# Kernel tuning notes

Measured on AMD Instinct MI355X. Metric: run time of the kernel, lower is better.

## Reference

```python
import jax, jax.numpy as jnp
import numpy as np

G, N_PER_G, V, H, DIN, DOUT, E = 1024, 64, 32, 128, 128, 10, 1048576
N = G * N_PER_G


def _lin(key, fan_in, fan_out):
    k1, k2 = jax.random.split(key)
    s = 1.0 / np.sqrt(fan_in)
    return (jax.random.uniform(k1, (fan_in, fan_out), jnp.float32, -s, s),
            jax.random.uniform(k2, (fan_out,), jnp.float32, -s, s))


def setup_inputs() -> dict:
    key = jax.random.key(0)
    ks = jax.random.split(key, 16)
    x = jax.random.normal(ks[0], (N, DIN), jnp.float32)
    # random edges constrained within each graph's contiguous node block
    gid = jax.random.randint(ks[1], (E,), 0, G)
    src = gid * N_PER_G + jax.random.randint(ks[2], (E,), 0, N_PER_G)
    dst = gid * N_PER_G + jax.random.randint(ks[3], (E,), 0, N_PER_G)
    edge_index = jnp.stack([src, dst]).astype(jnp.int64)
    batch = jnp.repeat(jnp.arange(G, dtype=jnp.int64), N_PER_G)
    edge_weights = jnp.ones((G, N_PER_G, V), jnp.float32) / V  # uniform init
    vemb = jax.random.normal(ks[4], (G, V, H), jnp.float32)
    vemb = vemb / jnp.linalg.norm(vemb, axis=-1, keepdims=True)
    W_emb, b_emb = _lin(ks[5], DIN, H)
    W_gcn, b_gcn = _lin(ks[6], H, H)
    aff_W1, aff_b1 = _lin(ks[7], H, H)
    aff_W2, aff_b2 = _lin(ks[8], H, H)
    vn_W1, vn_b1 = _lin(ks[9], H, H)
    vn_W2, vn_b2 = _lin(ks[10], H, H)
    mlp_W1, mlp_b1 = _lin(ks[11], H, H)
    mlp_W2, mlp_b2 = _lin(ks[12], H, DOUT)
    return dict(x=x, edge_index=edge_index, batch=batch, edge_weights=edge_weights,
                vemb=vemb, W_emb=W_emb, b_emb=b_emb, W_gcn=W_gcn, b_gcn=b_gcn,
                aff_W1=aff_W1, aff_b1=aff_b1, aff_W2=aff_W2, aff_b2=aff_b2,
                vn_W1=vn_W1, vn_b1=vn_b1, vn_W2=vn_W2, vn_b2=vn_b2,
                mlp_W1=mlp_W1, mlp_b1=mlp_b1, mlp_W2=mlp_W2, mlp_b2=mlp_b2)


def reference(x, edge_index, batch, edge_weights, vemb, W_emb, b_emb, W_gcn, b_gcn,
              aff_W1, aff_b1, aff_W2, aff_b2, vn_W1, vn_b1, vn_W2, vn_b2,
              mlp_W1, mlp_b1, mlp_W2, mlp_b2):
    n_nodes = x.shape[0]
    g, n, v = edge_weights.shape
    h = x @ W_emb + b_emb                                   # node embedding
    # GCNConv with self-loops and symmetric normalization
    hw = h @ W_gcn
    sl = jnp.arange(n_nodes)
    s = jnp.concatenate([edge_index[0], sl])
    d = jnp.concatenate([edge_index[1], sl])
    deg = jax.ops.segment_sum(jnp.ones_like(d, dtype=h.dtype), d, num_segments=n_nodes)
    inv = jax.lax.rsqrt(jnp.maximum(deg, 1.0))
    msg = hw[s] * (inv[s] * inv[d])[:, None]                # [E+N, H]
    h = jax.nn.relu(jax.ops.segment_sum(msg, d, num_segments=n_nodes) + b_gcn)
    # affinity MLP
    aff = jax.nn.relu(h @ aff_W1 + aff_b1) @ aff_W2 + aff_b2
    hg = h.reshape(g, n, -1)
    affg = aff.reshape(g, n, -1)
    # attention vs fixed normalized virtual-node embeddings
    att = jnp.einsum('gnh,gvh->gnv', affg, vemb) / jnp.sqrt(jnp.asarray(hg.shape[-1], h.dtype))
    ew = edge_weights * (1.0 + jax.nn.sigmoid(att))
    rs = ew.sum(axis=-1, keepdims=True)
    ew = ew / jnp.where(rs == 0, 1.0, rs)                   # row-normalize
    vn = jnp.einsum('gnv,gnh->gvh', ew, hg)                 # weighted scatter-pool
    vn = jax.nn.relu(vn @ vn_W1 + vn_b1) @ vn_W2 + vn_b2
    gf = vn.mean(axis=1)                                    # [G, H]
    return jax.nn.relu(gf @ mlp_W1 + mlp_b1) @ mlp_W2 + mlp_b2
```

## Files before the change

### kernel.cpp

```cpp
#include <hip/hip_runtime.h>
#include <hip/hip_bf16.h>
#include <cstddef>


#define EDGES 1048576
#define TS 72
#define AS 64
#define VS 136
#define BS 40

typedef __attribute__((ext_vector_type(8))) short short8;
typedef __attribute__((ext_vector_type(4))) float f32x4;
typedef __hip_bfloat16 bf;
struct __align__(8) bf4 { bf v[4]; };

__device__ __forceinline__ int foff(int nt, int ks, int l15, int kofs) {
    return (nt * 4 + ks) * 512 + l15 * 32 + kofs;
}

__device__ __forceinline__ short8 cvt8(const float* p) {
    float4 v0 = *(const float4*)p, v1 = *(const float4*)(p + 4);
    union { short8 v; bf e[8]; } u;
    u.e[0] = __float2bfloat16(v0.x); u.e[1] = __float2bfloat16(v0.y);
    u.e[2] = __float2bfloat16(v0.z); u.e[3] = __float2bfloat16(v0.w);
    u.e[4] = __float2bfloat16(v1.x); u.e[5] = __float2bfloat16(v1.y);
    u.e[6] = __float2bfloat16(v1.z); u.e[7] = __float2bfloat16(v1.w);
    return u.v;
}

__global__ __launch_bounds__(256) void prep(
    const float* __restrict__ vemb, const float* __restrict__ aff_b2,
    const float* __restrict__ aff_W2, const float* __restrict__ W_emb,
    const float* __restrict__ W_gcn, const float* __restrict__ b_emb,
    const float* __restrict__ aff_W1, const float* __restrict__ vn_W1,
    const float* __restrict__ vn_W2,
    bf* __restrict__ gWb, float* __restrict__ bfold,
    bf* __restrict__ gS, float* __restrict__ gbatt, unsigned* __restrict__ Cnt)
{
    const int b = blockIdx.x, t = threadIdx.x;
    const int wv = t >> 6, lane = t & 63, l15 = lane & 15, q = lane >> 4;
    const int kofs = q * 8;
    if (b < 1024) {
        __shared__ __align__(16) bf sV[32 * VS];
        const float4* gv = (const float4*)(vemb + (size_t)b * 4096);
#pragma unroll
        for (int tt = 0; tt < 4; ++tt) {
            int i = t + tt * 256;
            int v = i >> 5, o4 = i & 31;
            float4 w = gv[i];
            bf4 tv;
            tv.v[0] = __float2bfloat16(w.x); tv.v[1] = __float2bfloat16(w.y);
            tv.v[2] = __float2bfloat16(w.z); tv.v[3] = __float2bfloat16(w.w);
            *(bf4*)(sV + v * VS + o4 * 4) = tv;
        }
        __syncthreads();
        {
            int v = t >> 3, sg = t & 7;
            float s = 0.f;
            const bf* pv = sV + v * VS + sg * 16;
            const float* pb = aff_b2 + sg * 16;
#pragma unroll
            for (int o = 0; o < 16; ++o) s += pb[o] * __bfloat162float(pv[o]);
            s += __shfl_xor(s, 1); s += __shfl_xor(s, 2); s += __shfl_xor(s, 4);
            if (sg == 0) gbatt[b * 32 + v] = s;
        }
        {
            const int mt = wv & 1, nb = (wv >> 1) * 4;
            f32x4 acc[4] = {};
#pragma unroll
            for (int ks = 0; ks < 4; ++ks) {
                short8 a = *(const short8*)(sV + (mt * 16 + l15) * VS + ks * 32 + kofs);
#pragma unroll
                for (int nt = 0; nt < 4; ++nt) {
                    int n = (nb + nt) * 16 + l15;
                    short8 bb = cvt8(aff_W2 + n * 128 + ks * 32 + kofs);
                    acc[nt] = __builtin_amdgcn_mfma_f32_16x16x32_bf16(a, bb, acc[nt], 0, 0, 0);
                }
            }
#pragma unroll
            for (int nt = 0; nt < 4; ++nt)
#pragma unroll
                for (int r = 0; r < 4; ++r) {
                    int v = mt * 16 + q * 4 + r;
                    int k = (nb + nt) * 16 + l15;
                    int off = ((v >> 4) * 4 + (k >> 5)) * 512 + (v & 15) * 32 + (k & 31);
                    gS[(size_t)b * 4096 + off] = __float2bfloat16(acc[nt][r]);
                }
        }
    } else if (b == 1024) {
        if (t < 128) {
            float acc = 0.f;
#pragma unroll 16
            for (int m = 0; m < 128; ++m) acc = fmaf(b_emb[m], W_gcn[m * 128 + t], acc);
            bfold[t] = acc;
        }
#pragma unroll
        for (int kt2 = 0; kt2 < 2; ++kt2) {
            int kt = wv * 2 + kt2;
            short8 Af[4];
#pragma unroll
            for (int ks = 0; ks < 4; ++ks)
                Af[ks] = cvt8(W_emb + (kt * 16 + l15) * 128 + ks * 32 + kofs);
#pragma unroll
            for (int jt = 0; jt < 8; ++jt) {
                f32x4 acc = {};
#pragma unroll
                for (int ks = 0; ks < 4; ++ks) {
                    union { short8 v; bf e[8]; } u;
#pragma unroll
                    for (int i = 0; i < 8; ++i)
                        u.e[i] = __float2bfloat16(W_gcn[(ks * 32 + kofs + i) * 128 + jt * 16 + l15]);
                    acc = __builtin_amdgcn_mfma_f32_16x16x32_bf16(Af[ks], u.v, acc, 0, 0, 0);
                }
#pragma unroll
                for (int r = 0; r < 4; ++r) {
                    int k = kt * 16 + q * 4 + r;
                    gWb[(jt * 4 + (k >> 5)) * 512 + l15 * 32 + (k & 31)] =
                        __float2bfloat16(acc[r]);
                }
            }
        }
    } else if (b < 1028) {
        const float* src = (b == 1025) ? aff_W1 : (b == 1026) ? vn_W1 : vn_W2;
        bf* dst = gWb + (size_t)(b - 1024) * 16384;
        for (int i = t; i < 16384; i += 256) {
            int n = i >> 7, k = i & 127;
            int off = ((n >> 4) * 4 + (k >> 5)) * 512 + (n & 15) * 32 + (k & 31);
            dst[off] = __float2bfloat16(src[k * 128 + n]);
        }
    } else {
        for (int i = t; i < 1024; i += 256) Cnt[i] = 0u;
    }
}

__global__ __launch_bounds__(256) void scat(const int* __restrict__ ei,
                                            unsigned* __restrict__ Cnt,
                                            unsigned short* __restrict__ sorted)
{
    __shared__ unsigned lh[1024];
    __shared__ unsigned sBase[1024];
    int t = threadIdx.x, b = blockIdx.x;
    for (int i = t; i < 1024; i += 256) lh[i] = 0;
    __syncthreads();
    unsigned er[16];
    int base = b * 4096;
#pragma unroll
    for (int i = 0; i < 16; ++i) {
        int e = base + i * 256 + t;
        int s = ei[e], d = ei[EDGES + e];
        unsigned g = (unsigned)s >> 6;
        er[i] = (g << 12) | (unsigned)((d & 63) << 6) | (unsigned)(s & 63);
        atomicAdd(&lh[g], 1u);
    }
    __syncthreads();
    for (int i = t; i < 1024; i += 256) {
        unsigned c = lh[i];
        if (c) sBase[i] = atomicAdd(&Cnt[i], c);
    }
    __syncthreads();
    for (int i = t; i < 1024; i += 256) lh[i] = 0;
    __syncthreads();
#pragma unroll
    for (int i = 0; i < 16; ++i) {
        unsigned g = er[i] >> 12;
        unsigned r = atomicAdd(&lh[g], 1u);
        unsigned p = sBase[g] + r;
        if (p < 2048) sorted[(size_t)g * 2048 + p] = (unsigned short)(er[i] & 0xFFFu);
    }
}

__device__ __forceinline__ void gemmA8(const short8 A[4], const bf* __restrict__ gW,
                                       int l15, int kofs, f32x4 acc[8])
{
#pragma unroll
    for (int hf = 0; hf < 2; ++hf) {
        short8 b[4], bn[4];
#pragma unroll
        for (int nt = 0; nt < 4; ++nt)
            b[nt] = *(const short8*)(gW + foff(hf * 4 + nt, 0, l15, kofs));
#pragma unroll
        for (int ks = 0; ks < 4; ++ks) {
            if (ks < 3)
#pragma unroll
                for (int nt = 0; nt < 4; ++nt)
                    bn[nt] = *(const short8*)(gW + foff(hf * 4 + nt, ks + 1, l15, kofs));
#pragma unroll
            for (int nt = 0; nt < 4; ++nt)
                acc[hf * 4 + nt] = __builtin_amdgcn_mfma_f32_16x16x32_bf16(
                    A[ks], b[nt], acc[hf * 4 + nt], 0, 0, 0);
#pragma unroll
            for (int nt = 0; nt < 4; ++nt) b[nt] = bn[nt];
        }
    }
}

__device__ __forceinline__ void gemmA4(const short8 A[4], const bf* __restrict__ gW,
                                       int ntb, int l15, int kofs, f32x4 acc[4])
{
    short8 b[4], bn[4];
#pragma unroll
    for (int nt = 0; nt < 4; ++nt)
        b[nt] = *(const short8*)(gW + foff(ntb + nt, 0, l15, kofs));
#pragma unroll
    for (int ks = 0; ks < 4; ++ks) {
        if (ks < 3)
#pragma unroll
            for (int nt = 0; nt < 4; ++nt)
                bn[nt] = *(const short8*)(gW + foff(ntb + nt, ks + 1, l15, kofs));
#pragma unroll
        for (int nt = 0; nt < 4; ++nt)
            acc[nt] = __builtin_amdgcn_mfma_f32_16x16x32_bf16(A[ks], b[nt], acc[nt], 0, 0, 0);
#pragma unroll
        for (int nt = 0; nt < 4; ++nt) b[nt] = bn[nt];
    }
}

__device__ __forceinline__ void bounceA(const float vals[8][4], bf* slab,
                                        int q, int l15, short8 A[4])
{
#pragma unroll
    for (int ks = 0; ks < 4; ++ks) {
#pragma unroll
        for (int h = 0; h < 2; ++h)
#pragma unroll
            for (int r = 0; r < 4; ++r)
                slab[(q * 4 + r) * BS + h * 16 + l15] = __float2bfloat16(vals[ks * 2 + h][r]);
        A[ks] = *(const short8*)(slab + l15 * BS + q * 8);
    }
}

__global__ __launch_bounds__(256, 4) void fused_graph(
    const float* __restrict__ x, const float* __restrict__ edge_w,
    const bf* __restrict__ gWb, const float* __restrict__ bfold,
    const float* __restrict__ b_gcn, const float* __restrict__ aff_b1,
    const float* __restrict__ vn_b1, const float* __restrict__ vn_b2,
    const bf* __restrict__ gS, const float* __restrict__ gbatt,
    const float* __restrict__ mlp_W1, const float* __restrict__ mlp_b1,
    const float* __restrict__ mlp_W2, const float* __restrict__ mlp_b2,
    const unsigned short* __restrict__ sorted, const unsigned* __restrict__ Cnt,
    float* __restrict__ out)
{
    __shared__ __align__(16) bf sT [128 * TS];
    __shared__ __align__(16) bf sAdj[64 * AS];
    __shared__ __align__(16) bf sBounce[4 * 16 * BS];
    __shared__ __align__(16) bf sVn[32 * VS];
    __shared__ float sInv[64];

    const int tid = threadIdx.x;
    const int g = blockIdx.x;
    const int wv = tid >> 6;
    const int lane = tid & 63;
    const int l15 = lane & 15;
    const int q = lane >> 4;
    const int kofs = q * 8;
    bf* slab = sBounce + wv * (16 * BS);
    float* sGfp = (float*)sBounce;
    unsigned* cnt = (unsigned*)sVn;

    {
        uint4* c4 = (uint4*)cnt;
        c4[tid] = make_uint4(0, 0, 0, 0);
    }
    __syncthreads();
    {
        unsigned ecnt = Cnt[g]; if (ecnt > 2048) ecnt = 2048;
        const unsigned short* seg = sorted + (size_t)g * 2048;
        for (unsigned i = tid; i < ecnt; i += 256) {
            unsigned w = seg[i];
            atomicAdd(&cnt[(w >> 6) * 16 + ((w & 63u) >> 2)], 1u << ((w & 3u) * 8));
        }
    }
    __syncthreads();
    {
        int row = tid >> 2, q4 = tid & 3;
        float rs = 0.f;
#pragma unroll
        for (int w4 = 0; w4 < 4; ++w4) {
            unsigned wd = cnt[row * 16 + q4 * 4 + w4];
            bf4 tv;
#pragma unroll
            for (int j = 0; j < 4; ++j) {
                int c = (q4 * 4 + w4) * 4 + j;
                float v = (float)((wd >> (j * 8)) & 255u) + (c == row ? 1.f : 0.f);
                rs += v;
                tv.v[j] = __float2bfloat16(v);
            }
            *(bf4*)(sAdj + row * AS + (q4 * 4 + w4) * 4) = tv;
        }
        rs += __shfl_xor(rs, 1);
        rs += __shfl_xor(rs, 2);
        if (q4 == 0) sInv[row] = rsqrtf(rs);
    }
    __syncthreads();

    {
        const float4* xrow = (const float4*)(x + ((size_t)g * 64 + 16 * wv + l15) * 128);
        short8 A[4];
#pragma unroll
        for (int ks = 0; ks < 4; ++ks) {
            float4 a0 = xrow[ks * 8 + q * 2];
            float4 a1 = xrow[ks * 8 + q * 2 + 1];
            union { short8 v; bf e[8]; } u;
            u.e[0] = __float2bfloat16(a0.x); u.e[1] = __float2bfloat16(a0.y);
            u.e[2] = __float2bfloat16(a0.z); u.e[3] = __float2bfloat16(a0.w);
            u.e[4] = __float2bfloat16(a1.x); u.e[5] = __float2bfloat16(a1.y);
            u.e[6] = __float2bfloat16(a1.z); u.e[7] = __float2bfloat16(a1.w);
            A[ks] = u.v;
        }
        f32x4 acc[8] = {};
        gemmA8(A, gWb, l15, kofs, acc);
        float bf_[8];
#pragma unroll
        for (int nt = 0; nt < 8; ++nt) bf_[nt] = bfold[nt * 16 + l15];
        float iv[4];
#pragma unroll
        for (int r = 0; r < 4; ++r) iv[r] = sInv[16 * wv + q * 4 + r];
#pragma unroll
        for (int nt = 0; nt < 8; ++nt) {
            bf4 tv;
#pragma unroll
            for (int r = 0; r < 4; ++r)
                tv.v[r] = __float2bfloat16((acc[nt][r] + bf_[nt]) * iv[r]);
            *(bf4*)(sT + (nt * 16 + l15) * TS + 16 * wv + q * 4) = tv;
        }
    }
    __syncthreads();

    float hvals[8][4];
    {
        f32x4 acc[8] = {};
#pragma unroll
        for (int ks = 0; ks < 2; ++ks) {
            short8 a = *(const short8*)(sAdj + (16 * wv + l15) * AS + ks * 32 + kofs);
#pragma unroll
            for (int nt = 0; nt < 8; ++nt) {
                short8 bb = *(const short8*)(sT + (nt * 16 + l15) * TS + ks * 32 + kofs);
                acc[nt] = __builtin_amdgcn_mfma_f32_16x16x32_bf16(a, bb, acc[nt], 0, 0, 0);
            }
        }
        float iv[4];
#pragma unroll
        for (int r = 0; r < 4; ++r) iv[r] = sInv[16 * wv + q * 4 + r];
#pragma unroll
        for (int nt = 0; nt < 8; ++nt) {
            float bg = b_gcn[nt * 16 + l15];
#pragma unroll
            for (int r = 0; r < 4; ++r)
                hvals[nt][r] = fmaxf(acc[nt][r] * iv[r] + bg, 0.f);
        }
    }
    __syncthreads();

    short8 Ah[4];
    {
#pragma unroll
        for (int nt = 0; nt < 8; ++nt) {
            bf4 tv;
#pragma unroll
            for (int r = 0; r < 4; ++r) tv.v[r] = __float2bfloat16(hvals[nt][r]);
            *(bf4*)(sT + (nt * 16 + l15) * TS + 16 * wv + q * 4) = tv;
        }
        bounceA(hvals, slab, q, l15, Ah);
    }

    short8 Aa[4];
    {
        f32x4 acc[8] = {};
        gemmA8(Ah, gWb + 16384, l15, kofs, acc);
        float av[8][4];
#pragma unroll
        for (int nt = 0; nt < 8; ++nt) {
            float ba = aff_b1[nt * 16 + l15];
#pragma unroll
            for (int r = 0; r < 4; ++r) av[nt][r] = fmaxf(acc[nt][r] + ba, 0.f);
        }
        bounceA(av, slab, q, l15, Aa);
    }

    {
        short8 Sf[8];
#pragma unroll
        for (int nt = 0; nt < 2; ++nt)
#pragma unroll
            for (int ks = 0; ks < 4; ++ks)
                Sf[nt * 4 + ks] = *(const short8*)(gS + (size_t)g * 4096 + foff(nt, ks, l15, kofs));
        float ewv[2][4];
#pragma unroll
        for (int nt = 0; nt < 2; ++nt)
#pragma unroll
            for (int r = 0; r < 4; ++r)
                ewv[nt][r] = edge_w[(size_t)g * 2048 + (16 * wv + q * 4 + r) * 32 + nt * 16 + l15];
        float bt[2] = { gbatt[g * 32 + l15], gbatt[g * 32 + 16 + l15] };
        f32x4 acc[2] = {};
#pragma unroll
        for (int ks = 0; ks < 4; ++ks) {
            acc[0] = __builtin_amdgcn_mfma_f32_16x16x32_bf16(Aa[ks], Sf[ks],     acc[0], 0, 0, 0);
            acc[1] = __builtin_amdgcn_mfma_f32_16x16x32_bf16(Aa[ks], Sf[4 + ks], acc[1], 0, 0, 0);
        }
        const float sc = 0.08838834764831845f;
        float e[2][4];
#pragma unroll
        for (int r = 0; r < 4; ++r) {
#pragma unroll
            for (int nt = 0; nt < 2; ++nt) {
                float att = (acc[nt][r] + bt[nt]) * sc;
                e[nt][r] = ewv[nt][r] * (1.f + 1.f / (1.f + __expf(-att)));
            }
            float rs = e[0][r] + e[1][r];
            rs += __shfl_xor(rs, 1); rs += __shfl_xor(rs, 2);
            rs += __shfl_xor(rs, 4); rs += __shfl_xor(rs, 8);
            float ri = (rs == 0.f) ? 1.f : 1.f / rs;
            e[0][r] *= ri; e[1][r] *= ri;
        }
#pragma unroll
        for (int nt = 0; nt < 2; ++nt) {
            bf4 tv;
#pragma unroll
            for (int r = 0; r < 4; ++r) tv.v[r] = __float2bfloat16(e[nt][r]);
            *(bf4*)(sAdj + (nt * 16 + l15) * AS + 16 * wv + q * 4) = tv;
        }
    }
    __syncthreads();

    const int mb = wv & 1, hf = wv >> 1;
    {
        f32x4 acc[4] = {};
#pragma unroll
        for (int ks = 0; ks < 2; ++ks) {
            short8 a = *(const short8*)(sAdj + (mb * 16 + l15) * AS + ks * 32 + kofs);
#pragma unroll
            for (int nt = 0; nt < 4; ++nt) {
                short8 bb = *(const short8*)(sT + (hf * 64 + nt * 16 + l15) * TS + ks * 32 + kofs);
                acc[nt] = __builtin_amdgcn_mfma_f32_16x16x32_bf16(a, bb, acc[nt], 0, 0, 0);
            }
        }
#pragma unroll
        for (int nt = 0; nt < 4; ++nt)
#pragma unroll
            for (int r = 0; r < 4; ++r)
                sVn[(mb * 16 + q * 4 + r) * VS + hf * 64 + nt * 16 + l15] =
                    __float2bfloat16(acc[nt][r]);
    }
    __syncthreads();

    bf* vn1 = sT;
    {
        short8 A[4];
#pragma unroll
        for (int ks = 0; ks < 4; ++ks)
            A[ks] = *(const short8*)(sVn + (mb * 16 + l15) * VS + ks * 32 + kofs);
        f32x4 acc[4] = {};
        gemmA4(A, gWb + 2 * 16384, hf * 4, l15, kofs, acc);
#pragma unroll
        for (int nt = 0; nt < 4; ++nt) {
            float b1 = vn_b1[hf * 64 + nt * 16 + l15];
#pragma unroll
            for (int r = 0; r < 4; ++r)
                vn1[(mb * 16 + q * 4 + r) * VS + hf * 64 + nt * 16 + l15] =
                    __float2bfloat16(fmaxf(acc[nt][r] + b1, 0.f));
        }
    }
    __syncthreads();

    {
        short8 A[4];
#pragma unroll
        for (int ks = 0; ks < 4; ++ks)
            A[ks] = *(const short8*)(vn1 + (mb * 16 + l15) * VS + ks * 32 + kofs);
        f32x4 acc[4] = {};
        gemmA4(A, gWb + 3 * 16384, hf * 4, l15, kofs, acc);
#pragma unroll
        for (int nt = 0; nt < 4; ++nt) {
            float b2 = vn_b2[hf * 64 + nt * 16 + l15];
            float p = (acc[nt][0] + b2) + (acc[nt][1] + b2) + (acc[nt][2] + b2) + (acc[nt][3] + b2);
            p += __shfl_xor(p, 16);
            p += __shfl_xor(p, 32);
            if (q == 0) sGfp[mb * 128 + hf * 64 + nt * 16 + l15] = p;
        }
    }
    __syncthreads();
    if (tid < 128) sGfp[tid] = (sGfp[tid] + sGfp[128 + tid]) * 0.03125f;
    __syncthreads();
    if (tid < 128) {
        float a = mlp_b1[tid];
#pragma unroll 16
        for (int k = 0; k < 128; ++k) a = fmaf(sGfp[k], mlp_W1[k * 128 + tid], a);
        sGfp[128 + tid] = fmaxf(a, 0.f);
    }
    __syncthreads();
    if (tid < 160) {
        int o = tid >> 4, jg = tid & 15;
        float p = 0.f;
#pragma unroll
        for (int t2 = 0; t2 < 8; ++t2) {
            int j = jg * 8 + t2;
            p = fmaf(sGfp[128 + j], mlp_W2[j * 10 + o], p);
        }
        p += __shfl_xor(p, 1); p += __shfl_xor(p, 2);
        p += __shfl_xor(p, 4); p += __shfl_xor(p, 8);
        if (jg == 0) out[g * 10 + o] = p + mlp_b2[o];
    }
}

extern "C" void kernel_launch(void* const* d_in, const int* in_sizes, int n_in,
                              void* d_out, int out_size, void* d_ws, size_t ws_size,
                              hipStream_t stream)
{
    const float* x       = (const float*)d_in[0];
    const int*   ei      = (const int*)  d_in[1];
    const float* edge_w  = (const float*)d_in[3];
    const float* vemb    = (const float*)d_in[4];
    const float* W_emb   = (const float*)d_in[5];
    const float* b_emb   = (const float*)d_in[6];
    const float* W_gcn   = (const float*)d_in[7];
    const float* b_gcn   = (const float*)d_in[8];
    const float* aff_W1  = (const float*)d_in[9];
    const float* aff_b1  = (const float*)d_in[10];
    const float* aff_W2  = (const float*)d_in[11];
    const float* aff_b2  = (const float*)d_in[12];
    const float* vn_W1   = (const float*)d_in[13];
    const float* vn_b1   = (const float*)d_in[14];
    const float* vn_W2   = (const float*)d_in[15];
    const float* vn_b2   = (const float*)d_in[16];
    const float* mlp_W1  = (const float*)d_in[17];
    const float* mlp_b1  = (const float*)d_in[18];
    const float* mlp_W2  = (const float*)d_in[19];
    const float* mlp_b2  = (const float*)d_in[20];

    char* ws = (char*)d_ws;
    unsigned short* sorted = (unsigned short*)ws;
    unsigned* Cnt   = (unsigned*)(ws + (4u << 20));
    bf*       gWb   = (bf*)     (ws + (4u << 20) + 65536);
    float*    bfold = (float*)  (ws + (4u << 20) + 65536 + 131072);
    bf*       gS    = (bf*)     (ws + (5u << 20));
    float*    gbatt = (float*)  (ws + (13u << 20));

    prep<<<dim3(1029), dim3(256), 0, stream>>>(
        vemb, aff_b2, aff_W2, W_emb, W_gcn, b_emb, aff_W1, vn_W1, vn_W2,
        gWb, bfold, gS, gbatt, Cnt);
    scat<<<dim3(256), dim3(256), 0, stream>>>(ei, Cnt, sorted);
    fused_graph<<<dim3(1024), dim3(256), 0, stream>>>(
        x, edge_w, gWb, bfold, b_gcn, aff_b1, vn_b1, vn_b2,
        gS, gbatt, mlp_W1, mlp_b1, mlp_W2, mlp_b2, sorted, Cnt, (float*)d_out);
}
```

Measured before the change: 213.5 us.

## Fold per-graph vemb·aff_W2 precompute into fused kernel and merge prep with scatter

Moves the per-graph vemb×aff_W2 product and the bias-attention term out of the prep kernel and into the main fused_graph kernel, computed in shared memory. This removes the gS/gbatt global round-trip. The prep and scatter kernels are merged into one launch, with the counter reset done by a memset. x, vemb and edge_weight loads are issued early so they overlap the adjacency counting. The cost is extra MFMA work, more registers and more shared memory in the main kernel, which may lower occupancy.

```diff
diff --git a/kernel.cpp b/kernel.cpp
--- a/kernel.cpp
+++ b/kernel.cpp
@@ -6,7 +6,7 @@
 #define EDGES 1048576
 #define TS 72
 #define AS 64
-#define VS 136
+#define SS 136
 #define BS 40
 
 typedef __attribute__((ext_vector_type(8))) short short8;
@@ -28,66 +28,49 @@
     return u.v;
 }
 
-__global__ __launch_bounds__(256) void prep(
-    const float* __restrict__ vemb, const float* __restrict__ aff_b2,
-    const float* __restrict__ aff_W2, const float* __restrict__ W_emb,
-    const float* __restrict__ W_gcn, const float* __restrict__ b_emb,
-    const float* __restrict__ aff_W1, const float* __restrict__ vn_W1,
-    const float* __restrict__ vn_W2,
-    bf* __restrict__ gWb, float* __restrict__ bfold,
-    bf* __restrict__ gS, float* __restrict__ gbatt, unsigned* __restrict__ Cnt)
+__global__ __launch_bounds__(256) void k1(
+    const int* __restrict__ ei,
+    const float* __restrict__ W_emb, const float* __restrict__ W_gcn,
+    const float* __restrict__ b_emb, const float* __restrict__ aff_W1,
+    const float* __restrict__ vn_W1, const float* __restrict__ vn_W2,
+    const float* __restrict__ aff_W2,
+    unsigned* __restrict__ Cnt, unsigned short* __restrict__ sorted,
+    bf* __restrict__ gWb, bf* __restrict__ gW2f, float* __restrict__ bfold)
 {
     const int b = blockIdx.x, t = threadIdx.x;
-    const int wv = t >> 6, lane = t & 63, l15 = lane & 15, q = lane >> 4;
-    const int kofs = q * 8;
-    if (b < 1024) {
-        __shared__ __align__(16) bf sV[32 * VS];
-        const float4* gv = (const float4*)(vemb + (size_t)b * 4096);
-#pragma unroll
-        for (int tt = 0; tt < 4; ++tt) {
-            int i = t + tt * 256;
-            int v = i >> 5, o4 = i & 31;
-            float4 w = gv[i];
-            bf4 tv;
-            tv.v[0] = __float2bfloat16(w.x); tv.v[1] = __float2bfloat16(w.y);
-            tv.v[2] = __float2bfloat16(w.z); tv.v[3] = __float2bfloat16(w.w);
-            *(bf4*)(sV + v * VS + o4 * 4) = tv;
-        }
+    if (b < 256) {
+        __shared__ unsigned lh[1024];
+        __shared__ unsigned sBase[1024];
+        for (int i = t; i < 1024; i += 256) lh[i] = 0;
         __syncthreads();
-        {
-            int v = t >> 3, sg = t & 7;
-            float s = 0.f;
-            const bf* pv = sV + v * VS + sg * 16;
-            const float* pb = aff_b2 + sg * 16;
-#pragma unroll
-            for (int o = 0; o < 16; ++o) s += pb[o] * __bfloat162float(pv[o]);
-            s += __shfl_xor(s, 1); s += __shfl_xor(s, 2); s += __shfl_xor(s, 4);
-            if (sg == 0) gbatt[b * 32 + v] = s;
-        }
-        {
-            const int mt = wv & 1, nb = (wv >> 1) * 4;
-            f32x4 acc[4] = {};
-#pragma unroll
-            for (int ks = 0; ks < 4; ++ks) {
-                short8 a = *(const short8*)(sV + (mt * 16 + l15) * VS + ks * 32 + kofs);
-#pragma unroll
-                for (int nt = 0; nt < 4; ++nt) {
-                    int n = (nb + nt) * 16 + l15;
-                    short8 bb = cvt8(aff_W2 + n * 128 + ks * 32 + kofs);
-                    acc[nt] = __builtin_amdgcn_mfma_f32_16x16x32_bf16(a, bb, acc[nt], 0, 0, 0);
-                }
-            }
-#pragma unroll
-            for (int nt = 0; nt < 4; ++nt)
-#pragma unroll
-                for (int r = 0; r < 4; ++r) {
-                    int v = mt * 16 + q * 4 + r;
-                    int k = (nb + nt) * 16 + l15;
-                    int off = ((v >> 4) * 4 + (k >> 5)) * 512 + (v & 15) * 32 + (k & 31);
-                    gS[(size_t)b * 4096 + off] = __float2bfloat16(acc[nt][r]);
-                }
-        }
-    } else if (b == 1024) {
+        unsigned er[16];
+        int base = b * 4096;
+#pragma unroll
+        for (int i = 0; i < 16; ++i) {
+            int e = base + i * 256 + t;
+            int s = ei[e], d = ei[EDGES + e];
+            unsigned g = (unsigned)s >> 6;
+            er[i] = (g << 12) | (unsigned)((d & 63) << 6) | (unsigned)(s & 63);
+            atomicAdd(&lh[g], 1u);
+        }
+        __syncthreads();
+        for (int i = t; i < 1024; i += 256) {
+            unsigned c = lh[i];
+            if (c) sBase[i] = atomicAdd(&Cnt[i], c);
+        }
+        __syncthreads();
+        for (int i = t; i < 1024; i += 256) lh[i] = 0;
+        __syncthreads();
+#pragma unroll
+        for (int i = 0; i < 16; ++i) {
+            unsigned g = er[i] >> 12;
+            unsigned r = atomicAdd(&lh[g], 1u);
+            unsigned p = sBase[g] + r;
+            if (p < 2048) sorted[(size_t)g * 2048 + p] = (unsigned short)(er[i] & 0xFFFu);
+        }
+    } else if (b == 256) {
+        const int wv = t >> 6, lane = t & 63, l15 = lane & 15, q = lane >> 4;
+        const int kofs = q * 8;
         if (t < 128) {
             float acc = 0.f;
 #pragma unroll 16
@@ -120,52 +103,20 @@
                 }
             }
         }
-    } else if (b < 1028) {
-        const float* src = (b == 1025) ? aff_W1 : (b == 1026) ? vn_W1 : vn_W2;
-        bf* dst = gWb + (size_t)(b - 1024) * 16384;
+    } else if (b < 260) {
+        const float* src = (b == 257) ? aff_W1 : (b == 258) ? vn_W1 : vn_W2;
+        bf* dst = gWb + (size_t)(b - 256) * 16384;
         for (int i = t; i < 16384; i += 256) {
             int n = i >> 7, k = i & 127;
             int off = ((n >> 4) * 4 + (k >> 5)) * 512 + (n & 15) * 32 + (k & 31);
             dst[off] = __float2bfloat16(src[k * 128 + n]);
         }
     } else {
-        for (int i = t; i < 1024; i += 256) Cnt[i] = 0u;
-    }
-}
-
-__global__ __launch_bounds__(256) void scat(const int* __restrict__ ei,
-                                            unsigned* __restrict__ Cnt,
-                                            unsigned short* __restrict__ sorted)
-{
-    __shared__ unsigned lh[1024];
-    __shared__ unsigned sBase[1024];
-    int t = threadIdx.x, b = blockIdx.x;
-    for (int i = t; i < 1024; i += 256) lh[i] = 0;
-    __syncthreads();
-    unsigned er[16];
-    int base = b * 4096;
-#pragma unroll
-    for (int i = 0; i < 16; ++i) {
-        int e = base + i * 256 + t;
-        int s = ei[e], d = ei[EDGES + e];
-        unsigned g = (unsigned)s >> 6;
-        er[i] = (g << 12) | (unsigned)((d & 63) << 6) | (unsigned)(s & 63);
-        atomicAdd(&lh[g], 1u);
-    }
-    __syncthreads();
-    for (int i = t; i < 1024; i += 256) {
-        unsigned c = lh[i];
-        if (c) sBase[i] = atomicAdd(&Cnt[i], c);
-    }
-    __syncthreads();
-    for (int i = t; i < 1024; i += 256) lh[i] = 0;
-    __syncthreads();
-#pragma unroll
-    for (int i = 0; i < 16; ++i) {
-        unsigned g = er[i] >> 12;
-        unsigned r = atomicAdd(&lh[g], 1u);
-        unsigned p = sBase[g] + r;
-        if (p < 2048) sorted[(size_t)g * 2048 + p] = (unsigned short)(er[i] & 0xFFFu);
+        for (int i = t; i < 16384; i += 256) {
+            int n = i >> 7, k = i & 127;
+            int off = ((n >> 4) * 4 + (k >> 5)) * 512 + (n & 15) * 32 + (k & 31);
+            gW2f[off] = __float2bfloat16(aff_W2[n * 128 + k]);
+        }
     }
 }
 
@@ -231,10 +182,12 @@
 
 __global__ __launch_bounds__(256, 4) void fused_graph(
     const float* __restrict__ x, const float* __restrict__ edge_w,
-    const bf* __restrict__ gWb, const float* __restrict__ bfold,
+    const float* __restrict__ vemb,
+    const bf* __restrict__ gWb, const bf* __restrict__ gW2f,
+    const float* __restrict__ bfold,
     const float* __restrict__ b_gcn, const float* __restrict__ aff_b1,
+    const float* __restrict__ aff_b2,
     const float* __restrict__ vn_b1, const float* __restrict__ vn_b2,
-    const bf* __restrict__ gS, const float* __restrict__ gbatt,
     const float* __restrict__ mlp_W1, const float* __restrict__ mlp_b1,
     const float* __restrict__ mlp_W2, const float* __restrict__ mlp_b2,
     const unsigned short* __restrict__ sorted, const unsigned* __restrict__ Cnt,
@@ -242,9 +195,10 @@
 {
     __shared__ __align__(16) bf sT [128 * TS];
     __shared__ __align__(16) bf sAdj[64 * AS];
-    __shared__ __align__(16) bf sBounce[4 * 16 * BS];
-    __shared__ __align__(16) bf sVn[32 * VS];
+    __shared__ __align__(16) bf sB  [4 * 16 * BS];
+    __shared__ __align__(16) bf sSV [32 * SS];
     __shared__ float sInv[64];
+    __shared__ float sBatt[32];
 
     const int tid = threadIdx.x;
     const int g = blockIdx.x;
@@ -253,24 +207,63 @@
     const int l15 = lane & 15;
     const int q = lane >> 4;
     const int kofs = q * 8;
-    bf* slab = sBounce + wv * (16 * BS);
-    float* sGfp = (float*)sBounce;
-    unsigned* cnt = (unsigned*)sVn;
-
-    {
-        uint4* c4 = (uint4*)cnt;
-        c4[tid] = make_uint4(0, 0, 0, 0);
-    }
-    __syncthreads();
-    {
-        unsigned ecnt = Cnt[g]; if (ecnt > 2048) ecnt = 2048;
+    const int mt = wv & 1, hf = wv >> 1;
+    bf* slab = sB + wv * (16 * BS);
+    float* sGfp = (float*)sB;
+    unsigned* cnt = (unsigned*)sB;
+
+    unsigned ecnt = Cnt[g]; if (ecnt > 2048) ecnt = 2048;
+    short8 Ax[4];
+    {
+        const float* xrow = x + ((size_t)g * 64 + 16 * wv + l15) * 128;
+#pragma unroll
+        for (int ks = 0; ks < 4; ++ks) Ax[ks] = cvt8(xrow + ks * 32 + kofs);
+    }
+    short8 Avm[4];
+    {
+        const float* vrow = vemb + (size_t)g * 4096 + (mt * 16 + l15) * 128;
+#pragma unroll
+        for (int ks = 0; ks < 4; ++ks) Avm[ks] = cvt8(vrow + ks * 32 + kofs);
+    }
+    float ewreg[2][4];
+#pragma unroll
+    for (int nt = 0; nt < 2; ++nt)
+#pragma unroll
+        for (int r = 0; r < 4; ++r)
+            ewreg[nt][r] = edge_w[(size_t)g * 2048 + (16 * wv + q * 4 + r) * 32 + nt * 16 + l15];
+
+    ((uint4*)cnt)[tid] = make_uint4(0, 0, 0, 0);
+    __syncthreads();
+
+    {
         const unsigned short* seg = sorted + (size_t)g * 2048;
         for (unsigned i = tid; i < ecnt; i += 256) {
             unsigned w = seg[i];
             atomicAdd(&cnt[(w >> 6) * 16 + ((w & 63u) >> 2)], 1u << ((w & 3u) * 8));
         }
     }
-    __syncthreads();
+    {
+        f32x4 accS[4] = {};
+        gemmA4(Avm, gW2f, hf * 4, l15, kofs, accS);
+#pragma unroll
+        for (int nt = 0; nt < 4; ++nt)
+#pragma unroll
+            for (int r = 0; r < 4; ++r)
+                sSV[(mt * 16 + q * 4 + r) * SS + (hf * 4 + nt) * 16 + l15] =
+                    __float2bfloat16(accS[nt][r]);
+    }
+    {
+        int v = tid >> 3, sg = tid & 7;
+        const float* pv = vemb + (size_t)g * 4096 + v * 128 + sg * 16;
+        const float* pb = aff_b2 + sg * 16;
+        float s = 0.f;
+#pragma unroll
+        for (int o = 0; o < 16; ++o) s += pb[o] * pv[o];
+        s += __shfl_xor(s, 1); s += __shfl_xor(s, 2); s += __shfl_xor(s, 4);
+        if (sg == 0) sBatt[v] = s;
+    }
+    __syncthreads();
+
     {
         int row = tid >> 2, q4 = tid & 3;
         float rs = 0.f;
@@ -294,21 +287,8 @@
     __syncthreads();
 
     {
-        const float4* xrow = (const float4*)(x + ((size_t)g * 64 + 16 * wv + l15) * 128);
-        short8 A[4];
-#pragma unroll
-        for (int ks = 0; ks < 4; ++ks) {
-            float4 a0 = xrow[ks * 8 + q * 2];
-            float4 a1 = xrow[ks * 8 + q * 2 + 1];
-            union { short8 v; bf e[8]; } u;
-            u.e[0] = __float2bfloat16(a0.x); u.e[1] = __float2bfloat16(a0.y);
-            u.e[2] = __float2bfloat16(a0.z); u.e[3] = __float2bfloat16(a0.w);
-            u.e[4] = __float2bfloat16(a1.x); u.e[5] = __float2bfloat16(a1.y);
-            u.e[6] = __float2bfloat16(a1.z); u.e[7] = __float2bfloat16(a1.w);
-            A[ks] = u.v;
-        }
         f32x4 acc[8] = {};
-        gemmA8(A, gWb, l15, kofs, acc);
+        gemmA8(Ax, gWb, l15, kofs, acc);
         float bf_[8];
 #pragma unroll
         for (int nt = 0; nt < 8; ++nt) bf_[nt] = bfold[nt * 16 + l15];
@@ -378,33 +358,23 @@
     }
 
     {
-        short8 Sf[8];
-#pragma unroll
-        for (int nt = 0; nt < 2; ++nt)
-#pragma unroll
-            for (int ks = 0; ks < 4; ++ks)
-                Sf[nt * 4 + ks] = *(const short8*)(gS + (size_t)g * 4096 + foff(nt, ks, l15, kofs));
-        float ewv[2][4];
-#pragma unroll
-        for (int nt = 0; nt < 2; ++nt)
-#pragma unroll
-            for (int r = 0; r < 4; ++r)
-                ewv[nt][r] = edge_w[(size_t)g * 2048 + (16 * wv + q * 4 + r) * 32 + nt * 16 + l15];
-        float bt[2] = { gbatt[g * 32 + l15], gbatt[g * 32 + 16 + l15] };
         f32x4 acc[2] = {};
 #pragma unroll
         for (int ks = 0; ks < 4; ++ks) {
-            acc[0] = __builtin_amdgcn_mfma_f32_16x16x32_bf16(Aa[ks], Sf[ks],     acc[0], 0, 0, 0);
-            acc[1] = __builtin_amdgcn_mfma_f32_16x16x32_bf16(Aa[ks], Sf[4 + ks], acc[1], 0, 0, 0);
+            short8 s0 = *(const short8*)(sSV + l15 * SS + ks * 32 + kofs);
+            short8 s1 = *(const short8*)(sSV + (16 + l15) * SS + ks * 32 + kofs);
+            acc[0] = __builtin_amdgcn_mfma_f32_16x16x32_bf16(Aa[ks], s0, acc[0], 0, 0, 0);
+            acc[1] = __builtin_amdgcn_mfma_f32_16x16x32_bf16(Aa[ks], s1, acc[1], 0, 0, 0);
         }
         const float sc = 0.08838834764831845f;
+        float bt[2] = { sBatt[l15], sBatt[16 + l15] };
         float e[2][4];
 #pragma unroll
         for (int r = 0; r < 4; ++r) {
 #pragma unroll
             for (int nt = 0; nt < 2; ++nt) {
                 float att = (acc[nt][r] + bt[nt]) * sc;
-                e[nt][r] = ewv[nt][r] * (1.f + 1.f / (1.f + __expf(-att)));
+                e[nt][r] = ewreg[nt][r] * (1.f + 1.f / (1.f + __expf(-att)));
             }
             float rs = e[0][r] + e[1][r];
             rs += __shfl_xor(rs, 1); rs += __shfl_xor(rs, 2);
@@ -422,12 +392,11 @@
     }
     __syncthreads();
 
-    const int mb = wv & 1, hf = wv >> 1;
     {
         f32x4 acc[4] = {};
 #pragma unroll
         for (int ks = 0; ks < 2; ++ks) {
-            short8 a = *(const short8*)(sAdj + (mb * 16 + l15) * AS + ks * 32 + kofs);
+            short8 a = *(const short8*)(sAdj + (mt * 16 + l15) * AS + ks * 32 + kofs);
 #pragma unroll
             for (int nt = 0; nt < 4; ++nt) {
                 short8 bb = *(const short8*)(sT + (hf * 64 + nt * 16 + l15) * TS + ks * 32 + kofs);
@@ -438,7 +407,7 @@
         for (int nt = 0; nt < 4; ++nt)
 #pragma unroll
             for (int r = 0; r < 4; ++r)
-                sVn[(mb * 16 + q * 4 + r) * VS + hf * 64 + nt * 16 + l15] =
+                sSV[(mt * 16 + q * 4 + r) * SS + hf * 64 + nt * 16 + l15] =
                     __float2bfloat16(acc[nt][r]);
     }
     __syncthreads();
@@ -448,7 +417,7 @@
         short8 A[4];
 #pragma unroll
         for (int ks = 0; ks < 4; ++ks)
-            A[ks] = *(const short8*)(sVn + (mb * 16 + l15) * VS + ks * 32 + kofs);
+            A[ks] = *(const short8*)(sSV + (mt * 16 + l15) * SS + ks * 32 + kofs);
         f32x4 acc[4] = {};
         gemmA4(A, gWb + 2 * 16384, hf * 4, l15, kofs, acc);
 #pragma unroll
@@ -456,7 +425,7 @@
             float b1 = vn_b1[hf * 64 + nt * 16 + l15];
 #pragma unroll
             for (int r = 0; r < 4; ++r)
-                vn1[(mb * 16 + q * 4 + r) * VS + hf * 64 + nt * 16 + l15] =
+                vn1[(mt * 16 + q * 4 + r) * SS + hf * 64 + nt * 16 + l15] =
                     __float2bfloat16(fmaxf(acc[nt][r] + b1, 0.f));
         }
     }
@@ -466,7 +435,7 @@
         short8 A[4];
 #pragma unroll
         for (int ks = 0; ks < 4; ++ks)
-            A[ks] = *(const short8*)(vn1 + (mb * 16 + l15) * VS + ks * 32 + kofs);
+            A[ks] = *(const short8*)(vn1 + (mt * 16 + l15) * SS + ks * 32 + kofs);
         f32x4 acc[4] = {};
         gemmA4(A, gWb + 3 * 16384, hf * 4, l15, kofs, acc);
 #pragma unroll
@@ -475,7 +444,7 @@
             float p = (acc[nt][0] + b2) + (acc[nt][1] + b2) + (acc[nt][2] + b2) + (acc[nt][3] + b2);
             p += __shfl_xor(p, 16);
             p += __shfl_xor(p, 32);
-            if (q == 0) sGfp[mb * 128 + hf * 64 + nt * 16 + l15] = p;
+            if (q == 0) sGfp[mt * 128 + hf * 64 + nt * 16 + l15] = p;
         }
     }
     __syncthreads();
@@ -532,14 +501,14 @@
     unsigned* Cnt   = (unsigned*)(ws + (4u << 20));
     bf*       gWb   = (bf*)     (ws + (4u << 20) + 65536);
     float*    bfold = (float*)  (ws + (4u << 20) + 65536 + 131072);
-    bf*       gS    = (bf*)     (ws + (5u << 20));
-    float*    gbatt = (float*)  (ws + (13u << 20));
-
-    prep<<<dim3(1029), dim3(256), 0, stream>>>(
-        vemb, aff_b2, aff_W2, W_emb, W_gcn, b_emb, aff_W1, vn_W1, vn_W2,
-        gWb, bfold, gS, gbatt, Cnt);
-    scat<<<dim3(256), dim3(256), 0, stream>>>(ei, Cnt, sorted);
+    bf*       gW2f  = (bf*)     (ws + (4u << 20) + 262144);
+
+    hipMemsetAsync(Cnt, 0, 1024 * sizeof(unsigned), stream);
+    k1<<<dim3(261), dim3(256), 0, stream>>>(
+        ei, W_emb, W_gcn, b_emb, aff_W1, vn_W1, vn_W2, aff_W2,
+        Cnt, sorted, gWb, gW2f, bfold);
     fused_graph<<<dim3(1024), dim3(256), 0, stream>>>(
-        x, edge_w, gWb, bfold, b_gcn, aff_b1, vn_b1, vn_b2,
-        gS, gbatt, mlp_W1, mlp_b1, mlp_W2, mlp_b2, sorted, Cnt, (float*)d_out);
-}
+        x, edge_w, vemb, gWb, gW2f, bfold, b_gcn, aff_b1, aff_b2,
+        vn_b1, vn_b2, mlp_W1, mlp_b1, mlp_W2, mlp_b2,
+        sorted, Cnt, (float*)d_out);
+}
```

Result: faster. 196.6 us (-7.9%).
